# Optimization experiments

Measured on AMD Instinct MI355X. Metric: run time of the kernel, lower is better.

## Reference

```python
import jax, jax.numpy as jnp
import numpy as np


def setup_inputs() -> dict:
    key = jax.random.key(0)
    ks = jax.random.split(key, 5)
    B, S, D, L = 16, 256, 768, 32
    return {
        "head": jax.random.normal(ks[0], (B, S, D), dtype=jnp.float32),
        "dep": jax.random.normal(ks[1], (B, S, D), dtype=jnp.float32),
        "label_U_diag": jax.random.normal(ks[2], (L, D), dtype=jnp.float32) * 0.02,
        "label_W": jax.random.normal(ks[3], (L, 2 * D), dtype=jnp.float32) * 0.02,
        "label_b": jax.random.normal(ks[4], (L,), dtype=jnp.float32) * 0.02,
    }


def reference(head, dep, label_U_diag, label_W, label_b):
    # head, dep: [b, s, d]; label_U_diag: [l, d]; label_W: [l, 2d]; label_b: [l]
    d = head.shape[-1]
    # Bilinear term with diagonal U: t1[b,l,i,o] = sum_d head[b,i,d]*U[l,d]*dep[b,o,d]
    t1 = jnp.einsum('bid,ld,bod->blio', head, label_U_diag, dep)
    # Linear term: W @ concat(head_i, dep_o) = W_h @ head_i + W_d @ dep_o
    W_h, W_d = label_W[:, :d], label_W[:, d:]
    t2_h = jnp.einsum('ld,bid->bli', W_h, head)  # [b, l, s]
    t2_d = jnp.einsum('ld,bod->blo', W_d, dep)   # [b, l, s]
    return t1 + t2_h[:, :, :, None] + t2_d[:, :, None, :] + label_b[None, :, None, None]
```

## Files before the change

kernel.cpp:

```cpp
#include <hip/hip_runtime.h>
#include <hip/hip_bf16.h>
#include <stdint.h>


#define B_ 16
#define S_ 256
#define D_ 768
#define L_ 32
#define KQ_ (D_ / 8)
#define NT_ 12
#define NC_ 24

typedef unsigned short ushort_t;
typedef __attribute__((ext_vector_type(4))) float f32x4;
typedef __attribute__((ext_vector_type(8))) short s16x8;

__device__ __forceinline__ unsigned int pack_bf16(float f0, float f1) {
  unsigned int u0 = __builtin_bit_cast(unsigned int, f0) + 0x8000u;
  unsigned int u1 = __builtin_bit_cast(unsigned int, f1) + 0x8000u;
  return __builtin_amdgcn_perm(u1, u0, 0x07060302);
}

__global__ __launch_bounds__(256) void prep_kernel(
    const float* __restrict__ head, const float* __restrict__ dep,
    const float* __restrict__ labelW, ushort_t* __restrict__ depb,
    float* __restrict__ t2h, float* __restrict__ t2d) {
  const int wave = threadIdx.x >> 6;
  const int lane = threadIdx.x & 63;
  const int g = blockIdx.x * 4 + wave;
  const int sel = g >> 10;
  const int idx = g & 1023;
  const int b = idx >> 6;
  const int row0 = (idx & 63) * 4;
  const float* src = sel ? dep : head;
  float* t2x = sel ? t2d : t2h;
  const int d0 = lane * 12;

  float h[4][12];
  const float* rp = src + ((size_t)(b * S_ + row0)) * D_ + d0;
#pragma unroll
  for (int r = 0; r < 4; ++r) {
    float4 v0 = *(const float4*)(rp + (size_t)r * D_);
    float4 v1 = *(const float4*)(rp + (size_t)r * D_ + 4);
    float4 v2 = *(const float4*)(rp + (size_t)r * D_ + 8);
    h[r][0] = v0.x; h[r][1] = v0.y; h[r][2] = v0.z; h[r][3] = v0.w;
    h[r][4] = v1.x; h[r][5] = v1.y; h[r][6] = v1.z; h[r][7] = v1.w;
    h[r][8] = v2.x; h[r][9] = v2.y; h[r][10] = v2.z; h[r][11] = v2.w;
  }
  if (sel) {
    const size_t bb = (size_t)b * (KQ_ * S_ * 8);
    const int m = lane >> 1;
#pragma unroll
    for (int r = 0; r < 4; ++r) {
      const int col = row0 + r;
      unsigned int q0 = pack_bf16(h[r][0], h[r][1]);
      unsigned int q1 = pack_bf16(h[r][2], h[r][3]);
      unsigned int q2 = pack_bf16(h[r][4], h[r][5]);
      unsigned int q3 = pack_bf16(h[r][6], h[r][7]);
      unsigned int q4 = pack_bf16(h[r][8], h[r][9]);
      unsigned int q5 = pack_bf16(h[r][10], h[r][11]);
      if ((lane & 1) == 0) {
        uint4 a = {q0, q1, q2, q3};
        uint2 c = {q4, q5};
        *(uint4*)(depb + bb + ((size_t)(3 * m) * S_ + col) * 8) = a;
        *(uint2*)(depb + bb + ((size_t)(3 * m + 1) * S_ + col) * 8) = c;
      } else {
        uint2 c = {q0, q1};
        uint4 a = {q2, q3, q4, q5};
        *(uint2*)(depb + bb + ((size_t)(3 * m + 1) * S_ + col) * 8 + 4) = c;
        *(uint4*)(depb + bb + ((size_t)(3 * m + 2) * S_ + col) * 8) = a;
      }
    }
  }
  const float* wbase = labelW + sel * D_ + d0;
  for (int c = 0; c < 2; ++c) {
    float v[64];
#pragma unroll
    for (int j = 0; j < 64; ++j) v[j] = 0.f;
    const float* wc = wbase + (size_t)(c * 16) * (2 * D_);
#pragma unroll
    for (int lq = 0; lq < 16; ++lq) {
      const float* wp = wc + (size_t)lq * (2 * D_);
      float4 w0 = *(const float4*)(wp);
      float4 w1 = *(const float4*)(wp + 4);
      float4 w2 = *(const float4*)(wp + 8);
      float w[12] = {w0.x, w0.y, w0.z, w0.w, w1.x, w1.y, w1.z, w1.w,
                     w2.x, w2.y, w2.z, w2.w};
#pragma unroll
      for (int j = 0; j < 12; ++j) {
        v[lq * 4 + 0] += h[0][j] * w[j];
        v[lq * 4 + 1] += h[1][j] * w[j];
        v[lq * 4 + 2] += h[2][j] * w[j];
        v[lq * 4 + 3] += h[3][j] * w[j];
      }
    }
#pragma unroll
    for (int off = 32; off >= 1; off >>= 1) {
      const bool hi = (lane & off) != 0;
#pragma unroll
      for (int k = 0; k < 64; ++k) {
        if (k >= off) continue;
        float send = hi ? v[k] : v[k + off];
        float keep = hi ? v[k + off] : v[k];
        v[k] = keep + __shfl_xor(send, off);
      }
    }
    t2x[((size_t)(b * L_ + c * 16 + (lane >> 2))) * S_ + row0 + (lane & 3)] =
        v[0];
  }
}


#define SWZ(o) ((o) ^ ((((o) >> 10) & 3) << 4))

__global__ __launch_bounds__(256, 2) void main_kernel(
    const float* __restrict__ head, const ushort_t* __restrict__ depb,
    const float* __restrict__ U, const float* __restrict__ bias,
    const float* __restrict__ t2h, const float* __restrict__ t2d,
    float* __restrict__ out) {
  __shared__ __attribute__((aligned(16))) ushort_t As[2 * 2 * 4096];
  __shared__ float T2[384];

  const int hw = blockIdx.x;
  const int bid = ((hw & 7) << 7) | (hw >> 3);
  const int ic = bid & 1;
  const int bl = bid >> 1;
  const int l = bl & (L_ - 1);
  const int b = bl >> 5;
  const int ti = ic * 128;
  const int t = threadIdx.x;
  const int lane = t & 63;
  const int wave = t >> 6;

  for (int i = t; i < 384; i += 256)
    T2[i] = (i < 128) ? t2h[((size_t)(b * L_ + l)) * S_ + ti + i]
                      : t2d[((size_t)(b * L_ + l)) * S_ + (i - 128)];
  const float bv = bias[l];

  const int row0 = t >> 2;
  const int kg = t & 3;
  const float* hp0 = head + ((size_t)(b * S_ + ti + row0)) * D_ + kg * 8;
  const float* hp1 = hp0 + (size_t)64 * D_;
  const float* Up = U + (size_t)l * D_ + kg * 8;
  const int awo0s = SWZ((kg * 128 + row0) * 8);
  const int awo1s = awo0s + 512;

  const int aros = SWZ(((lane >> 4) * 128 + (lane & 15)) * 8);

  const ushort_t* dfb = depb + (size_t)b * (KQ_ * S_ * 8) +
                        ((size_t)((lane >> 4) * 256 + wave * 64 + (lane & 15))) * 8;

  f32x4 acc[8][4];
#pragma unroll
  for (int i = 0; i < 8; ++i)
#pragma unroll
    for (int j = 0; j < 4; ++j) acc[i][j] = {0.f, 0.f, 0.f, 0.f};

  s16x8 bfA[4], bfB[4];

#define LOAD_HU(ku)                                                           \
    float4 h0 = *(const float4*)(hp0 + (ku) * 32);                            \
    float4 h1 = *(const float4*)(hp0 + (ku) * 32 + 4);                        \
    float4 h2 = *(const float4*)(hp1 + (ku) * 32);                            \
    float4 h3 = *(const float4*)(hp1 + (ku) * 32 + 4);                        \
    float4 u0 = *(const float4*)(Up + (ku) * 32);                             \
    float4 u1 = *(const float4*)(Up + (ku) * 32 + 4);

#define PACK_WRITE_A(DST)                                                     \
  {                                                                           \
    uint4 w0, w1;                                                             \
    w0.x = pack_bf16(h0.x * u0.x, h0.y * u0.y);                               \
    w0.y = pack_bf16(h0.z * u0.z, h0.w * u0.w);                               \
    w0.z = pack_bf16(h1.x * u1.x, h1.y * u1.y);                               \
    w0.w = pack_bf16(h1.z * u1.z, h1.w * u1.w);                               \
    w1.x = pack_bf16(h2.x * u0.x, h2.y * u0.y);                               \
    w1.y = pack_bf16(h2.z * u0.z, h2.w * u0.w);                               \
    w1.z = pack_bf16(h3.x * u1.x, h3.y * u1.y);                               \
    w1.w = pack_bf16(h3.z * u1.z, h3.w * u1.w);                               \
    *(uint4*)((DST) + awo0s) = w0;                                            \
    *(uint4*)((DST) + awo1s) = w1;                                            \
  }

  {
    {
      LOAD_HU(0)
      PACK_WRITE_A(As)
    }
    {
      LOAD_HU(1)
      PACK_WRITE_A(As + 4096)
    }
#pragma unroll
    for (int ct = 0; ct < 4; ++ct)
      bfA[ct] = *(const s16x8*)(dfb + ct * 128);
  }
  asm volatile("s_waitcnt lgkmcnt(0)" ::: "memory");
  __builtin_amdgcn_s_barrier();
  __builtin_amdgcn_sched_barrier(0);

  int cur = 0;
  for (int tt = 0; tt < NT_; ++tt) {
    const ushort_t* pr = As + cur * 8192;
    ushort_t* pw = As + (cur ^ 1) * 8192;
    {
      int cb = 2 * tt + 1;
      const ushort_t* dfn = dfb + (size_t)cb * 8192;
#pragma unroll
      for (int ct = 0; ct < 4; ++ct)
        bfB[ct] = *(const s16x8*)(dfn + ct * 128);
      int ks = 2 * tt + 2;
      if (ks >= NC_) ks -= NC_;
      LOAD_HU(ks)
      __builtin_amdgcn_sched_barrier(0);
      s16x8 af[8];
#pragma unroll
      for (int rt = 0; rt < 8; ++rt)
        af[rt] = *(const s16x8*)(pr + aros + rt * 128);
      __builtin_amdgcn_s_setprio(1);
#pragma unroll
      for (int rt = 0; rt < 8; ++rt)
#pragma unroll
        for (int ct = 0; ct < 4; ++ct)
          acc[rt][ct] = __builtin_amdgcn_mfma_f32_16x16x32_bf16(
              af[rt], bfA[ct], acc[rt][ct], 0, 0, 0);
      __builtin_amdgcn_s_setprio(0);
      PACK_WRITE_A(pw)
    }
    {
      int cb = 2 * tt + 2;
      if (cb >= NC_) cb -= NC_;
      const ushort_t* dfn = dfb + (size_t)cb * 8192;
#pragma unroll
      for (int ct = 0; ct < 4; ++ct)
        bfA[ct] = *(const s16x8*)(dfn + ct * 128);
      int ks = 2 * tt + 3;
      if (ks >= NC_) ks -= NC_;
      LOAD_HU(ks)
      __builtin_amdgcn_sched_barrier(0);
      s16x8 af[8];
#pragma unroll
      for (int rt = 0; rt < 8; ++rt)
        af[rt] = *(const s16x8*)(pr + 4096 + aros + rt * 128);
      __builtin_amdgcn_s_setprio(1);
#pragma unroll
      for (int rt = 0; rt < 8; ++rt)
#pragma unroll
        for (int ct = 0; ct < 4; ++ct)
          acc[rt][ct] = __builtin_amdgcn_mfma_f32_16x16x32_bf16(
              af[rt], bfB[ct], acc[rt][ct], 0, 0, 0);
      __builtin_amdgcn_s_setprio(0);
      PACK_WRITE_A(pw + 4096)
    }
    asm volatile("s_waitcnt lgkmcnt(0)" ::: "memory");
    __builtin_amdgcn_s_barrier();
    __builtin_amdgcn_sched_barrier(0);
    cur ^= 1;
  }
#undef LOAD_HU
#undef PACK_WRITE_A

  const int colg = lane & 15;
  const int rgrp = lane >> 4;
  float* ob = out + (((size_t)(b * L_ + l)) * S_ + ti) * S_;
#pragma unroll
  for (int rt = 0; rt < 8; ++rt) {
    const int r0 = rt * 16 + rgrp * 4;
#pragma unroll
    for (int ct = 0; ct < 4; ++ct) {
      const int c = wave * 64 + ct * 16 + colg;
      const float addc = T2[128 + c] + bv;
      float* p = ob + (size_t)r0 * S_ + c;
#pragma unroll
      for (int r = 0; r < 4; ++r)
        p[(size_t)r * S_] = acc[rt][ct][r] + T2[r0 + r] + addc;
    }
  }
}

extern "C" void kernel_launch(void* const* d_in, const int* in_sizes, int n_in,
                              void* d_out, int out_size, void* d_ws, size_t ws_size,
                              hipStream_t stream) {
  const float* head = (const float*)d_in[0];
  const float* dep = (const float*)d_in[1];
  const float* U = (const float*)d_in[2];
  const float* W = (const float*)d_in[3];
  const float* bias = (const float*)d_in[4];
  float* out = (float*)d_out;

  ushort_t* depb = (ushort_t*)d_ws;
  float* t2h = (float*)((char*)d_ws + (size_t)B_ * S_ * D_ * 2);
  float* t2d = t2h + (size_t)B_ * L_ * S_;

  prep_kernel<<<512, 256, 0, stream>>>(head, dep, W, depb, t2h, t2d);
  main_kernel<<<B_ * L_ * 2, 256, 0, stream>>>(head, depb, U, bias, t2h, t2d, out);
}
```

Baseline: 214.5 us.

## Remap waves to a 2x2 grid of 64x128 output subtiles

Changes the per-wave tile from 128 rows x 64 columns to 64 rows x 128 columns, with the four waves arranged as a 2x2 grid. Each wave now reads half as many A fragments from LDS and twice as many B fragments straight from global memory per k-step, so the A-side LDS traffic drops while the global/L2 load per wave grows. It also raises register use for the B fragments, which may pressure occupancy at two blocks per CU.

Measured after the change: 224.1 us. 1.04x slower.

```diff
diff --git a/kernel.cpp b/kernel.cpp
--- a/kernel.cpp
+++ b/kernel.cpp
@@ -131,6 +131,8 @@
   const int t = threadIdx.x;
   const int lane = t & 63;
   const int wave = t >> 6;
+  const int wr = wave >> 1;
+  const int wc = wave & 1;
 
   for (int i = t; i < 384; i += 256)
     T2[i] = (i < 128) ? t2h[((size_t)(b * L_ + l)) * S_ + ti + i]
@@ -145,18 +147,19 @@
   const int awo0s = SWZ((kg * 128 + row0) * 8);
   const int awo1s = awo0s + 512;
 
-  const int aros = SWZ(((lane >> 4) * 128 + (lane & 15)) * 8);
-
-  const ushort_t* dfb = depb + (size_t)b * (KQ_ * S_ * 8) +
-                        ((size_t)((lane >> 4) * 256 + wave * 64 + (lane & 15))) * 8;
-
-  f32x4 acc[8][4];
-#pragma unroll
-  for (int i = 0; i < 8; ++i)
-#pragma unroll
-    for (int j = 0; j < 4; ++j) acc[i][j] = {0.f, 0.f, 0.f, 0.f};
-
-  s16x8 bfA[4], bfB[4];
+  const int aros = SWZ(((lane >> 4) * 128 + (lane & 15)) * 8) + wr * 512;
+
+  const ushort_t* dfb =
+      depb + (size_t)b * (KQ_ * S_ * 8) +
+      ((size_t)((lane >> 4) * 256 + wc * 128 + (lane & 15))) * 8;
+
+  f32x4 acc[4][8];
+#pragma unroll
+  for (int i = 0; i < 4; ++i)
+#pragma unroll
+    for (int j = 0; j < 8; ++j) acc[i][j] = {0.f, 0.f, 0.f, 0.f};
+
+  s16x8 bfA[8], bfB[8];
 
 #define LOAD_HU(ku)                                                           \
     float4 h0 = *(const float4*)(hp0 + (ku) * 32);                            \
@@ -181,6 +184,21 @@
     *(uint4*)((DST) + awo1s) = w1;                                            \
   }
 
+#define LOAD_BF(DSTB, chunk)                                                  \
+  {                                                                           \
+    const ushort_t* dfn = dfb + (size_t)(chunk) * 8192;                       \
+    _Pragma("unroll") for (int ct = 0; ct < 8; ++ct)                          \
+        DSTB[ct] = *(const s16x8*)(dfn + ct * 128);                           \
+  }
+
+#define MFMA16(AFB, BFB)                                                      \
+  {                                                                           \
+    _Pragma("unroll") for (int rt = 0; rt < 4; ++rt)                          \
+      _Pragma("unroll") for (int ct = 0; ct < 8; ++ct)                        \
+          acc[rt][ct] = __builtin_amdgcn_mfma_f32_16x16x32_bf16(              \
+              AFB[rt], BFB[ct], acc[rt][ct], 0, 0, 0);                        \
+  }
+
   {
     {
       LOAD_HU(0)
@@ -190,9 +208,7 @@
       LOAD_HU(1)
       PACK_WRITE_A(As + 4096)
     }
-#pragma unroll
-    for (int ct = 0; ct < 4; ++ct)
-      bfA[ct] = *(const s16x8*)(dfb + ct * 128);
+    LOAD_BF(bfA, 0)
   }
   asm volatile("s_waitcnt lgkmcnt(0)" ::: "memory");
   __builtin_amdgcn_s_barrier();
@@ -203,51 +219,34 @@
     const ushort_t* pr = As + cur * 8192;
     ushort_t* pw = As + (cur ^ 1) * 8192;
     {
-      int cb = 2 * tt + 1;
-      const ushort_t* dfn = dfb + (size_t)cb * 8192;
-#pragma unroll
-      for (int ct = 0; ct < 4; ++ct)
-        bfB[ct] = *(const s16x8*)(dfn + ct * 128);
+      LOAD_BF(bfB, 2 * tt + 1)
       int ks = 2 * tt + 2;
       if (ks >= NC_) ks -= NC_;
       LOAD_HU(ks)
       __builtin_amdgcn_sched_barrier(0);
-      s16x8 af[8];
-#pragma unroll
-      for (int rt = 0; rt < 8; ++rt)
+      s16x8 af[4];
+#pragma unroll
+      for (int rt = 0; rt < 4; ++rt)
         af[rt] = *(const s16x8*)(pr + aros + rt * 128);
       __builtin_amdgcn_s_setprio(1);
-#pragma unroll
-      for (int rt = 0; rt < 8; ++rt)
-#pragma unroll
-        for (int ct = 0; ct < 4; ++ct)
-          acc[rt][ct] = __builtin_amdgcn_mfma_f32_16x16x32_bf16(
-              af[rt], bfA[ct], acc[rt][ct], 0, 0, 0);
+      MFMA16(af, bfA)
       __builtin_amdgcn_s_setprio(0);
       PACK_WRITE_A(pw)
     }
     {
       int cb = 2 * tt + 2;
       if (cb >= NC_) cb -= NC_;
-      const ushort_t* dfn = dfb + (size_t)cb * 8192;
-#pragma unroll
-      for (int ct = 0; ct < 4; ++ct)
-        bfA[ct] = *(const s16x8*)(dfn + ct * 128);
+      LOAD_BF(bfA, cb)
       int ks = 2 * tt + 3;
       if (ks >= NC_) ks -= NC_;
       LOAD_HU(ks)
       __builtin_amdgcn_sched_barrier(0);
-      s16x8 af[8];
-#pragma unroll
-      for (int rt = 0; rt < 8; ++rt)
+      s16x8 af[4];
+#pragma unroll
+      for (int rt = 0; rt < 4; ++rt)
         af[rt] = *(const s16x8*)(pr + 4096 + aros + rt * 128);
       __builtin_amdgcn_s_setprio(1);
-#pragma unroll
-      for (int rt = 0; rt < 8; ++rt)
-#pragma unroll
-        for (int ct = 0; ct < 4; ++ct)
-          acc[rt][ct] = __builtin_amdgcn_mfma_f32_16x16x32_bf16(
-              af[rt], bfB[ct], acc[rt][ct], 0, 0, 0);
+      MFMA16(af, bfB)
       __builtin_amdgcn_s_setprio(0);
       PACK_WRITE_A(pw + 4096)
     }
@@ -258,21 +257,23 @@
   }
 #undef LOAD_HU
 #undef PACK_WRITE_A
+#undef LOAD_BF
+#undef MFMA16
 
   const int colg = lane & 15;
   const int rgrp = lane >> 4;
-  float* ob = out + (((size_t)(b * L_ + l)) * S_ + ti) * S_;
-#pragma unroll
-  for (int rt = 0; rt < 8; ++rt) {
+  float* ob = out + (((size_t)(b * L_ + l)) * S_ + ti + wr * 64) * S_ + wc * 128;
+#pragma unroll
+  for (int rt = 0; rt < 4; ++rt) {
     const int r0 = rt * 16 + rgrp * 4;
 #pragma unroll
-    for (int ct = 0; ct < 4; ++ct) {
-      const int c = wave * 64 + ct * 16 + colg;
-      const float addc = T2[128 + c] + bv;
+    for (int ct = 0; ct < 8; ++ct) {
+      const int c = ct * 16 + colg;
+      const float addc = T2[128 + wc * 128 + c] + bv;
       float* p = ob + (size_t)r0 * S_ + c;
 #pragma unroll
       for (int r = 0; r < 4; ++r)
-        p[(size_t)r * S_] = acc[rt][ct][r] + T2[r0 + r] + addc;
+        p[(size_t)r * S_] = acc[rt][ct][r] + T2[wr * 64 + r0 + r] + addc;
     }
   }
 }
```
